# Optimization experiments

Measured on AMD Instinct MI355X. Metric: run time of the kernel, lower is better.

Reference implementation:

```python
import jax, jax.numpy as jnp
import numpy as np
import math

L, H, E, D = 4, 8, 256, 32  # layers, heads, embed, head_dim
SCALE = 1.0 / math.sqrt(D)

def _ln(x, w, b, eps=1e-5):
    mu = jnp.mean(x, -1, keepdims=True)
    var = jnp.mean((x - mu) ** 2, -1, keepdims=True)
    return (x - mu) * jax.lax.rsqrt(var + eps) * w + b

def setup_inputs() -> dict:
    key = jax.random.key(0)
    ks = jax.random.split(key, 16)
    B, S, C = 32, 512, 512
    w = lambda k, sh: jax.random.normal(k, sh, jnp.float32) * 0.05
    return {
        'cnn_features': jax.random.normal(ks[0], (B, S, C), jnp.float32),
        'cnn_w': w(ks[1], (E, C)), 'cnn_b': jnp.zeros((E,), jnp.float32),
        'tok_emb': w(ks[2], (2, E)),
        'Wq': w(ks[3], (L, E, E)), 'bq': jnp.zeros((L, E), jnp.float32),
        'Wk': w(ks[4], (L, E, E)), 'bk': jnp.zeros((L, E), jnp.float32),
        'Wv': w(ks[5], (L, E, E)), 'bv': jnp.zeros((L, E), jnp.float32),
        'Wo': w(ks[6], (L, E, E)), 'bo': jnp.zeros((L, E), jnp.float32),
        'ln1_w': jnp.ones((L, E), jnp.float32), 'ln1_b': jnp.zeros((L, E), jnp.float32),
        'ln2_w': jnp.ones((L, E), jnp.float32), 'ln2_b': jnp.zeros((L, E), jnp.float32),
        'mlp_w1': w(ks[7], (L, 3 * E, E)), 'mlp_b1': jnp.zeros((L, 3 * E), jnp.float32),
        'mlp_w2': w(ks[8], (L, E, 3 * E)), 'mlp_b2': jnp.zeros((L, E), jnp.float32),
        'lnf_w': jnp.ones((E,), jnp.float32), 'lnf_b': jnp.zeros((E,), jnp.float32),
        'out_w1': w(ks[9], (2 * E, E)), 'out_b1': jnp.zeros((2 * E,), jnp.float32),
        'out_w2': w(ks[10], (C, 2 * E)), 'out_b2': jnp.zeros((C,), jnp.float32),
    }

def _forward(cnn_features, cnn_w, cnn_b, tok_emb, Wq, bq, Wk, bk, Wv, bv, Wo, bo,
             ln1_w, ln1_b, ln2_w, ln2_b, mlp_w1, mlp_b1, mlp_w2, mlp_b2,
             lnf_w, lnf_b, out_w1, out_b1, out_w2, out_b2):
    B, S, _ = cnn_features.shape
    # CNN feature projection + token-type embedding (all tokens type 0)
    x = cnn_features @ cnn_w.T + cnn_b + tok_emb[0]  # [B,S,E]
    for i in range(L):
        q = (x @ Wq[i].T + bq[i]).reshape(B, S, H, D).transpose(0, 2, 1, 3)
        k = (x @ Wk[i].T + bk[i]).reshape(B, S, H, D).transpose(0, 2, 1, 3)
        v = (x @ Wv[i].T + bv[i]).reshape(B, S, H, D).transpose(0, 2, 1, 3)
        scores = jnp.einsum('bhqd,bhkd->bhqk', q, k) * SCALE
        attn = jax.nn.softmax(scores, axis=-1)  # dropout = identity (eval)
        attended = jnp.einsum('bhqk,bhkd->bhqd', attn, v)
        attended = attended.transpose(0, 2, 1, 3).reshape(B, S, E)
        attn_out = attended @ Wo[i].T + bo[i]
        x = _ln(x + attn_out, ln1_w[i], ln1_b[i])
        h = jax.nn.gelu(x @ mlp_w1[i].T + mlp_b1[i], approximate=False)
        mlp_out = h @ mlp_w2[i].T + mlp_b2[i]
        x = _ln(x + mlp_out, ln2_w[i], ln2_b[i])
    x = _ln(x, lnf_w, lnf_b)
    h = jax.nn.gelu(x @ out_w1.T + out_b1, approximate=False)
    out = jax.nn.relu(h @ out_w2.T + out_b2)  # [B,S,cnn_feature_dim]
    return out

def reference(cnn_features, cnn_w, cnn_b, tok_emb, Wq, bq, Wk, bk, Wv, bv, Wo, bo,
              ln1_w, ln1_b, ln2_w, ln2_b, mlp_w1, mlp_b1, mlp_w2, mlp_b2,
              lnf_w, lnf_b, out_w1, out_b1, out_w2, out_b2):
    return _forward(cnn_features, cnn_w, cnn_b, tok_emb, Wq, bq, Wk, bk, Wv, bv, Wo, bo,
                    ln1_w, ln1_b, ln2_w, ln2_b, mlp_w1, mlp_b1, mlp_w2, mlp_b2,
                    lnf_w, lnf_b, out_w1, out_b1, out_w2, out_b2)
```

## Files before the change

kernel.cpp:

```cpp
#include <hip/hip_runtime.h>
#include <hip/hip_bf16.h>
#include <math.h>

#define B_SZ 32
#define S_SZ 512
#define C_SZ 512
#define E_SZ 256
#define H_SZ 8
#define D_SZ 32
#define L_SZ 4
#define N_TOK (B_SZ * S_SZ)
#define HID 768
#define MB (1048576)

typedef __attribute__((ext_vector_type(8))) short bf16x8;
typedef __attribute__((ext_vector_type(4))) float f32x4_t;

__device__ __forceinline__ float gelu_f(float x) {
    return 0.5f * x * (1.0f + erff(x * 0.70710678118654752f));
}

__device__ __forceinline__ ushort f2bf(float f) {
    uint u = __float_as_uint(f);
    return (ushort)((u + 0x7FFFu + ((u >> 16) & 1u)) >> 16);
}
__device__ __forceinline__ uint pack2(float a, float b) {
    __hip_bfloat162 h = __float22bfloat162_rn(make_float2(a, b));
    union { __hip_bfloat162 h; uint u; } c; c.h = h;
    return c.u;
}
__device__ __forceinline__ void unpack8(uint4 u, float* f) {
    f[0] = __uint_as_float((u.x & 0xFFFFu) << 16); f[1] = __uint_as_float(u.x & 0xFFFF0000u);
    f[2] = __uint_as_float((u.y & 0xFFFFu) << 16); f[3] = __uint_as_float(u.y & 0xFFFF0000u);
    f[4] = __uint_as_float((u.z & 0xFFFFu) << 16); f[5] = __uint_as_float(u.z & 0xFFFF0000u);
    f[6] = __uint_as_float((u.w & 0xFFFFu) << 16); f[7] = __uint_as_float(u.w & 0xFFFF0000u);
}

__device__ __forceinline__ void gload16(const ushort* g, ushort* l) {
    __builtin_amdgcn_global_load_lds(
        (const __attribute__((address_space(1))) void*)g,
        (__attribute__((address_space(3))) void*)l, 16, 0, 0);
}

__global__ __launch_bounds__(256)
void cvt_kernel(const float* __restrict__ src, ushort* __restrict__ dst)
{
    const int i = (blockIdx.x * 256 + threadIdx.x) * 8;
    const float4 a = *(const float4*)(src + i);
    const float4 b = *(const float4*)(src + i + 4);
    uint4 o;
    o.x = pack2(a.x, a.y); o.y = pack2(a.z, a.w);
    o.z = pack2(b.x, b.y); o.w = pack2(b.z, b.w);
    *(uint4*)(dst + i) = o;
}

__global__ __launch_bounds__(256)
void wcvt_kernel(const float* __restrict__ cnn_w, const float* __restrict__ Wo,
                 const float* __restrict__ Wq, const float* __restrict__ Wk,
                 const float* __restrict__ Wv, const float* __restrict__ mw1,
                 const float* __restrict__ mw2, const float* __restrict__ ow1,
                 const float* __restrict__ ow2, ushort* __restrict__ wb)
{
    const int i = (blockIdx.x * 256 + threadIdx.x) * 8;
    const float* src;
    if (i < 131072)       src = cnn_w + i;
    else if (i < 393216)  src = Wo + (i - 131072);
    else if (i < 1179648) {
        const int r = i - 393216;
        const int layer = r / 196608, rem = r % 196608;
        const int sub = rem >> 16, off = rem & 65535;
        src = (sub == 0 ? Wq : sub == 1 ? Wk : Wv) + layer * 65536 + off;
    }
    else if (i < 1966080) src = mw1 + (i - 1179648);
    else if (i < 2752512) src = mw2 + (i - 1966080);
    else if (i < 2883584) src = ow1 + (i - 2752512);
    else                  src = ow2 + (i - 2883584);
    const float4 a = *(const float4*)src;
    const float4 b = *(const float4*)(src + 4);
    uint4 o;
    o.x = pack2(a.x, a.y); o.y = pack2(a.z, a.w);
    o.z = pack2(b.x, b.y); o.w = pack2(b.z, b.w);
    *(uint4*)(wb + i) = o;
}

__global__ __launch_bounds__(256)
void bqkv_kernel(const float* __restrict__ bq, const float* __restrict__ bk,
                 const float* __restrict__ bv, float* __restrict__ dst)
{
    const int idx = blockIdx.x * 256 + threadIdx.x;
    const int layer = idx / 768, j = idx % 768;
    float v = (j < 256) ? bq[layer * 256 + j]
            : (j < 512) ? bk[layer * 256 + j - 256]
                        : bv[layer * 256 + j - 512];
    dst[layer * 768 + j] = v;
}

template<int ACT, int EPI, bool OF, bool OB>
__global__ __launch_bounds__(256)
void gemm_bf16_kernel(const ushort* __restrict__ A, const ushort* __restrict__ W,
                      const float* __restrict__ bias, const float* __restrict__ bias2,
                      float* __restrict__ Cf, ushort* __restrict__ Cb,
                      ushort* __restrict__ Cb2, int M, int K, int F)
{
    __shared__ __align__(16) ushort As[2][128 * 64];
    __shared__ __align__(16) ushort Bs[2][64 * 64];
    const int tid = threadIdx.x;
    const int bm = blockIdx.x * 128, bn = blockIdx.y * 64;
    const int lane = tid & 63, w = tid >> 6;
    const int lr8 = lane >> 3, lseg = lane & 7;
    const int lsx = lseg ^ lr8;
    const int wm = w >> 1, wn = w & 1;
    const int fr = lane & 15, fk = lane >> 4;
    const int fx = fr & 7;
    f32x4_t acc[4][2] = {};

    const ushort* Ag = A + (size_t)(bm + w * 32 + lr8) * K + lsx * 8;
    const ushort* Wg = W + (size_t)(bn + w * 16 + lr8) * K + lsx * 8;

    #pragma unroll
    for (int q = 0; q < 4; ++q) gload16(Ag + (size_t)q * 8 * K, &As[0][(w * 32 + q * 8) * 64]);
    #pragma unroll
    for (int q = 0; q < 2; ++q) gload16(Wg + (size_t)q * 8 * K, &Bs[0][(w * 16 + q * 8) * 64]);
    __syncthreads();

    const int NT = K >> 6;
    int cur = 0;
    for (int t = 0; t < NT; ++t) {
        if (t + 1 < NT) {
            const size_t k0 = (size_t)(t + 1) << 6;
            #pragma unroll
            for (int q = 0; q < 4; ++q)
                gload16(Ag + (size_t)q * 8 * K + k0, &As[cur ^ 1][(w * 32 + q * 8) * 64]);
            #pragma unroll
            for (int q = 0; q < 2; ++q)
                gload16(Wg + (size_t)q * 8 * K + k0, &Bs[cur ^ 1][(w * 16 + q * 8) * 64]);
        }
        bf16x8 af[2][4], bw[2][2];
        #pragma unroll
        for (int kk = 0; kk < 2; ++kk) {
            const int rs = ((kk * 4 + fk) ^ fx) * 8;
            #pragma unroll
            for (int i = 0; i < 4; ++i)
                af[kk][i] = *(const bf16x8*)&As[cur][(wm * 64 + i * 16 + fr) * 64 + rs];
            #pragma unroll
            for (int j = 0; j < 2; ++j)
                bw[kk][j] = *(const bf16x8*)&Bs[cur][(wn * 32 + j * 16 + fr) * 64 + rs];
        }
        #pragma unroll
        for (int kk = 0; kk < 2; ++kk)
            #pragma unroll
            for (int i = 0; i < 4; ++i)
                #pragma unroll
                for (int j = 0; j < 2; ++j)
                    acc[i][j] = __builtin_amdgcn_mfma_f32_16x16x32_bf16(af[kk][i], bw[kk][j], acc[i][j], 0, 0, 0);
        __syncthreads();
        cur ^= 1;
    }

    #pragma unroll
    for (int j = 0; j < 2; ++j) {
        const int col = bn + wn * 32 + j * 16 + fr;
        float bb = bias[col];
        if (bias2) bb += bias2[col];
        #pragma unroll
        for (int i = 0; i < 4; ++i) {
            #pragma unroll
            for (int r = 0; r < 4; ++r) {
                const int row = bm + wm * 64 + i * 16 + fk * 4 + r;
                float t = acc[i][j][r] + bb;
                if (ACT == 1) t = gelu_f(t);
                if (ACT == 2) t = fmaxf(t, 0.0f);
                if (EPI == 1) {
                    const int b2 = row >> 9, s2 = row & 511;
                    if (col < 512) {
                        Cb[(size_t)row * 512 + col] = f2bf(t);
                    } else {
                        const int cc = col - 512;
                        Cb2[(size_t)(((b2 << 3) + (cc >> 5)) << 14) + ((cc & 31) << 9) + s2] = f2bf(t);
                    }
                } else {
                    if (OF) Cf[(size_t)row * F + col] = t;
                    if (OB) Cb[(size_t)row * F + col] = f2bf(t);
                }
            }
        }
    }
}

__global__ __launch_bounds__(512)
void gemm_ln_kernel(const ushort* __restrict__ A, const ushort* __restrict__ W,
                    const float* __restrict__ bias, float* __restrict__ x,
                    ushort* __restrict__ xb, const float* __restrict__ lnw,
                    const float* __restrict__ lnb, int K)
{
    __shared__ __align__(16) ushort As[2][64 * 64];
    __shared__ __align__(16) ushort Bs[2][256 * 64];
    __shared__ float psum[64][8], psq[64][8], murs[64][2];
    const int tid = threadIdx.x;
    const int bm = blockIdx.x * 64;
    const int lane = tid & 63, w = tid >> 6;
    const int lr8 = lane >> 3, lseg = lane & 7;
    const int lsx = lseg ^ lr8;
    const int fr = lane & 15, fk = lane >> 4;
    const int fx = fr & 7;
    f32x4_t acc[4][2] = {};

    const ushort* Ag = A + (size_t)(bm + w * 8 + lr8) * K + lsx * 8;
    const ushort* Wg = W + (size_t)(w * 32 + lr8) * K + lsx * 8;

    gload16(Ag, &As[0][(w * 8) * 64]);
    #pragma unroll
    for (int q = 0; q < 4; ++q) gload16(Wg + (size_t)q * 8 * K, &Bs[0][(w * 32 + q * 8) * 64]);
    __syncthreads();

    const int NT = K >> 6;
    int cur = 0;
    for (int t = 0; t < NT; ++t) {
        if (t + 1 < NT) {
            const size_t k0 = (size_t)(t + 1) << 6;
            gload16(Ag + k0, &As[cur ^ 1][(w * 8) * 64]);
            #pragma unroll
            for (int q = 0; q < 4; ++q)
                gload16(Wg + (size_t)q * 8 * K + k0, &Bs[cur ^ 1][(w * 32 + q * 8) * 64]);
        }
        bf16x8 af[2][4], bw[2][2];
        #pragma unroll
        for (int kk = 0; kk < 2; ++kk) {
            const int rs = ((kk * 4 + fk) ^ fx) * 8;
            #pragma unroll
            for (int i = 0; i < 4; ++i)
                af[kk][i] = *(const bf16x8*)&As[cur][(i * 16 + fr) * 64 + rs];
            #pragma unroll
            for (int j = 0; j < 2; ++j)
                bw[kk][j] = *(const bf16x8*)&Bs[cur][(w * 32 + j * 16 + fr) * 64 + rs];
        }
        #pragma unroll
        for (int kk = 0; kk < 2; ++kk)
            #pragma unroll
            for (int i = 0; i < 4; ++i)
                #pragma unroll
                for (int j = 0; j < 2; ++j)
                    acc[i][j] = __builtin_amdgcn_mfma_f32_16x16x32_bf16(af[kk][i], bw[kk][j], acc[i][j], 0, 0, 0);
        __syncthreads();
        cur ^= 1;
    }

    float y[4][2][4];
    #pragma unroll
    for (int j = 0; j < 2; ++j) {
        const int col = w * 32 + j * 16 + fr;
        const float bb = bias[col];
        #pragma unroll
        for (int i = 0; i < 4; ++i)
            #pragma unroll
            for (int r = 0; r < 4; ++r) {
                const int row = i * 16 + fk * 4 + r;
                y[i][j][r] = acc[i][j][r] + bb + x[(size_t)(bm + row) * 256 + col];
            }
    }
    #pragma unroll
    for (int i = 0; i < 4; ++i)
        #pragma unroll
        for (int r = 0; r < 4; ++r) {
            float s = y[i][0][r] + y[i][1][r];
            float q = y[i][0][r] * y[i][0][r] + y[i][1][r] * y[i][1][r];
            #pragma unroll
            for (int off = 1; off < 16; off <<= 1) {
                s += __shfl_xor(s, off);
                q += __shfl_xor(q, off);
            }
            if (fr == 0) {
                psum[i * 16 + fk * 4 + r][w] = s;
                psq [i * 16 + fk * 4 + r][w] = q;
            }
        }
    __syncthreads();
    if (tid < 64) {
        float ms = 0.f, mq = 0.f;
        #pragma unroll
        for (int ww = 0; ww < 8; ++ww) { ms += psum[tid][ww]; mq += psq[tid][ww]; }
        const float mu = ms * (1.0f / 256.0f);
        const float var = mq * (1.0f / 256.0f) - mu * mu;
        murs[tid][0] = mu;
        murs[tid][1] = rsqrtf(var + 1e-5f);
    }
    __syncthreads();
    #pragma unroll
    for (int i = 0; i < 4; ++i)
        #pragma unroll
        for (int r = 0; r < 4; ++r) {
            const int row = i * 16 + fk * 4 + r;
            const float mu = murs[row][0], rs = murs[row][1];
            #pragma unroll
            for (int j = 0; j < 2; ++j) {
                const int col = w * 32 + j * 16 + fr;
                const float xn = (y[i][j][r] - mu) * rs * lnw[col] + lnb[col];
                x [(size_t)(bm + row) * 256 + col] = xn;
                xb[(size_t)(bm + row) * 256 + col] = f2bf(xn);
            }
        }
}

__global__ __launch_bounds__(512)
void attn_v4(const ushort* __restrict__ qk, const ushort* __restrict__ vt,
             ushort* __restrict__ out)
{
    __shared__ __align__(16) ushort Ks[512 * 40];
    __shared__ __align__(16) ushort Vs[32 * 520];
    const int bh = blockIdx.x;
    const int b = bh >> 3, h = bh & 7;
    const int tid = threadIdx.x;
    const int w = tid >> 6, lane = tid & 63;
    const int g = lane >> 4, c = lane & 15;

    #pragma unroll
    for (int i = 0; i < 4; ++i) {
        const int idx = tid + i * 512;
        const int kr = idx >> 2, seg = idx & 3;
        const uint4 kv = *(const uint4*)(qk + ((size_t)b * 512 + kr) * 512
                                         + 256 + h * 32 + seg * 8);
        const int p = (((kr >> 2) & 1) << 4) | (((kr >> 3) & 3) << 2) | (kr & 3);
        const int pos = (kr & ~31) | p;
        *(uint4*)&Ks[pos * 40 + seg * 8] = kv;
        const int dr = idx >> 6, vseg = idx & 63;
        const uint4 vv = *(const uint4*)(vt + (size_t)bh * 16384 + dr * 512 + vseg * 8);
        *(uint4*)&Vs[dr * 520 + vseg * 8] = vv;
    }

    bf16x8 qf[4];
    #pragma unroll
    for (int j = 0; j < 4; ++j) {
        const size_t qrow = (size_t)b * 512 + (j * 8 + w) * 16 + c;
        const uint4 qv = *(const uint4*)(qk + qrow * 512 + h * 32 + g * 8);
        float f[8]; unpack8(qv, f);
        const float scale = 0.17677669529663689f;
        union { uint u[4]; bf16x8 v; } qq;
        #pragma unroll
        for (int t = 0; t < 4; ++t) qq.u[t] = pack2(f[2*t] * scale, f[2*t+1] * scale);
        qf[j] = qq.v;
    }
    __syncthreads();

    const f32x4_t zz = {0.f, 0.f, 0.f, 0.f};
    #pragma unroll
    for (int j = 0; j < 4; ++j) {
        float m = -INFINITY, l = 0.f;
        f32x4_t o0 = zz, o1 = zz;
        for (int kt = 0; kt < 4; ++kt) {
            const int kbase = kt * 128;
            f32x4_t s[8];
            __builtin_amdgcn_s_setprio(1);
            #pragma unroll
            for (int kf = 0; kf < 8; ++kf) {
                const bf16x8 kfrag = *(const bf16x8*)&Ks[(kbase + kf * 16 + c) * 40 + g * 8];
                s[kf] = __builtin_amdgcn_mfma_f32_16x16x32_bf16(kfrag, qf[j], zz, 0, 0, 0);
            }
            __builtin_amdgcn_s_setprio(0);

            float mt = s[0][0];
            #pragma unroll
            for (int kf = 0; kf < 8; ++kf)
                #pragma unroll
                for (int r = 0; r < 4; ++r) mt = fmaxf(mt, s[kf][r]);
            mt = fmaxf(mt, __shfl_xor(mt, 16));
            mt = fmaxf(mt, __shfl_xor(mt, 32));
            const float mn = fmaxf(m, mt);
            const float corr = __expf(m - mn);
            m = mn;
            float lt = 0.f;
            #pragma unroll
            for (int kf = 0; kf < 8; ++kf)
                #pragma unroll
                for (int r = 0; r < 4; ++r) {
                    const float p = __expf(s[kf][r] - mn);
                    s[kf][r] = p; lt += p;
                }
            lt += __shfl_xor(lt, 16);
            lt += __shfl_xor(lt, 32);
            l = l * corr + lt;
            #pragma unroll
            for (int r = 0; r < 4; ++r) { o0[r] *= corr; o1[r] *= corr; }

            #pragma unroll
            for (int t = 0; t < 4; ++t) {
                union { uint u[4]; bf16x8 v; } pf;
                pf.u[0] = pack2(s[2*t][0],   s[2*t][1]);
                pf.u[1] = pack2(s[2*t][2],   s[2*t][3]);
                pf.u[2] = pack2(s[2*t+1][0], s[2*t+1][1]);
                pf.u[3] = pack2(s[2*t+1][2], s[2*t+1][3]);
                const bf16x8 va0 = *(const bf16x8*)&Vs[c * 520 + kbase + t * 32 + g * 8];
                const bf16x8 va1 = *(const bf16x8*)&Vs[(16 + c) * 520 + kbase + t * 32 + g * 8];
                __builtin_amdgcn_s_setprio(1);
                o0 = __builtin_amdgcn_mfma_f32_16x16x32_bf16(va0, pf.v, o0, 0, 0, 0);
                o1 = __builtin_amdgcn_mfma_f32_16x16x32_bf16(va1, pf.v, o1, 0, 0, 0);
                __builtin_amdgcn_s_setprio(0);
            }
        }

        const float inv = 1.0f / l;
        const size_t obase = ((size_t)b * 512 + (j * 8 + w) * 16 + c) * 256 + h * 32;
        ushort4 w0, w1;
        w0.x = f2bf(o0[0] * inv); w0.y = f2bf(o0[1] * inv);
        w0.z = f2bf(o0[2] * inv); w0.w = f2bf(o0[3] * inv);
        w1.x = f2bf(o1[0] * inv); w1.y = f2bf(o1[1] * inv);
        w1.z = f2bf(o1[2] * inv); w1.w = f2bf(o1[3] * inv);
        *(ushort4*)(out + obase + g * 4)      = w0;
        *(ushort4*)(out + obase + 16 + g * 4) = w1;
    }
}

__global__ __launch_bounds__(256)
void lnf_kernel(const float* __restrict__ x, const float* __restrict__ w,
                const float* __restrict__ b, ushort* __restrict__ xb)
{
    const int lane = threadIdx.x & 63;
    const int wv = threadIdx.x >> 6;
    const size_t row = (size_t)blockIdx.x * 4 + wv;
    const float4 val = *(const float4*)(x + row * E_SZ + lane * 4);
    float s  = val.x + val.y + val.z + val.w;
    float ss = val.x * val.x + val.y * val.y + val.z * val.z + val.w * val.w;
    #pragma unroll
    for (int off = 1; off < 64; off <<= 1) {
        s  += __shfl_xor(s, off, 64);
        ss += __shfl_xor(ss, off, 64);
    }
    const float mu  = s * (1.0f / 256.0f);
    const float var = ss * (1.0f / 256.0f) - mu * mu;
    const float rs  = rsqrtf(var + 1e-5f);
    const float4 wv4 = *(const float4*)(w + lane * 4);
    const float4 bv4 = *(const float4*)(b + lane * 4);
    ushort4 ob;
    ob.x = f2bf((val.x - mu) * rs * wv4.x + bv4.x);
    ob.y = f2bf((val.y - mu) * rs * wv4.y + bv4.y);
    ob.z = f2bf((val.z - mu) * rs * wv4.z + bv4.z);
    ob.w = f2bf((val.w - mu) * rs * wv4.w + bv4.w);
    *(ushort4*)(xb + row * E_SZ + lane * 4) = ob;
}

extern "C" void kernel_launch(void* const* d_in, const int* in_sizes, int n_in,
                              void* d_out, int out_size, void* d_ws, size_t ws_size,
                              hipStream_t stream)
{
    const float* cnn   = (const float*)d_in[0];
    const float* cnn_w = (const float*)d_in[1];
    const float* cnn_b = (const float*)d_in[2];
    const float* tok   = (const float*)d_in[3];
    const float* Wq    = (const float*)d_in[4];
    const float* bq    = (const float*)d_in[5];
    const float* Wk    = (const float*)d_in[6];
    const float* bk    = (const float*)d_in[7];
    const float* Wv    = (const float*)d_in[8];
    const float* bv    = (const float*)d_in[9];
    const float* Wo    = (const float*)d_in[10];
    const float* bo    = (const float*)d_in[11];
    const float* ln1w  = (const float*)d_in[12];
    const float* ln1b  = (const float*)d_in[13];
    const float* ln2w  = (const float*)d_in[14];
    const float* ln2b  = (const float*)d_in[15];
    const float* mw1   = (const float*)d_in[16];
    const float* mb1   = (const float*)d_in[17];
    const float* mw2   = (const float*)d_in[18];
    const float* mb2   = (const float*)d_in[19];
    const float* lnfw  = (const float*)d_in[20];
    const float* lnfb  = (const float*)d_in[21];
    const float* ow1   = (const float*)d_in[22];
    const float* ob1   = (const float*)d_in[23];
    const float* ow2   = (const float*)d_in[24];
    const float* ob2   = (const float*)d_in[25];

    const int M = N_TOK;
    char* ws = (char*)d_ws;

    float*  x     = (float*)(ws + 0);
    ushort* xb    = (ushort*)(ws + 16 * MB);
    ushort* qkb   = (ushort*)(ws + 24 * MB);
    ushort* cnnb  = (ushort*)(ws + 24 * MB);
    ushort* vt    = (ushort*)(ws + 40 * MB);
    ushort* ab_   = (ushort*)(ws + 48 * MB);
    ushort* hb_   = (ushort*)(ws + 40 * MB);
    ushort* wb    = (ushort*)(ws + 64 * MB);

    ushort* cnn_wb = wb;
    ushort* Wob    = wb + 131072;
    ushort* wqkv   = wb + 393216;
    ushort* mw1b   = wb + 1179648;
    ushort* mw2b   = wb + 1966080;
    ushort* ow1b   = wb + 2752512;
    ushort* ow2b   = wb + 2883584;
    float*  bqkv   = (float*)(ws + 64 * MB + 6291456);

    cvt_kernel<<<dim3(4096), dim3(256), 0, stream>>>(cnn, cnnb);
    wcvt_kernel<<<dim3(1536), dim3(256), 0, stream>>>(
        cnn_w, Wo, Wq, Wk, Wv, mw1, mw2, ow1, ow2, wb);
    bqkv_kernel<<<dim3(12), dim3(256), 0, stream>>>(bq, bk, bv, bqkv);

    gemm_bf16_kernel<0, 0, true, true><<<dim3(M / 128, E_SZ / 64), dim3(256), 0, stream>>>(
        cnnb, cnn_wb, cnn_b, tok, x, xb, nullptr, M, C_SZ, E_SZ);

    for (int i = 0; i < L_SZ; ++i) {
        gemm_bf16_kernel<0, 1, false, false><<<dim3(M / 128, HID / 64), dim3(256), 0, stream>>>(
            xb, wqkv + (size_t)i * 196608, bqkv + (size_t)i * 768, nullptr,
            nullptr, qkb, vt, M, E_SZ, HID);

        attn_v4<<<dim3(B_SZ * H_SZ), dim3(512), 0, stream>>>(qkb, vt, ab_);

        gemm_ln_kernel<<<dim3(M / 64), dim3(512), 0, stream>>>(
            ab_, Wob + (size_t)i * 65536, bo + (size_t)i * E_SZ,
            x, xb, ln1w + (size_t)i * E_SZ, ln1b + (size_t)i * E_SZ, E_SZ);

        gemm_bf16_kernel<1, 0, false, true><<<dim3(M / 128, HID / 64), dim3(256), 0, stream>>>(
            xb, mw1b + (size_t)i * HID * E_SZ, mb1 + (size_t)i * HID, nullptr,
            nullptr, hb_, nullptr, M, E_SZ, HID);

        gemm_ln_kernel<<<dim3(M / 64), dim3(512), 0, stream>>>(
            hb_, mw2b + (size_t)i * E_SZ * HID, mb2 + (size_t)i * E_SZ,
            x, xb, ln2w + (size_t)i * E_SZ, ln2b + (size_t)i * E_SZ, HID);
    }

    lnf_kernel<<<dim3(M / 4), dim3(256), 0, stream>>>(x, lnfw, lnfb, xb);

    gemm_bf16_kernel<1, 0, false, true><<<dim3(M / 128, (2 * E_SZ) / 64), dim3(256), 0, stream>>>(
        xb, ow1b, ob1, nullptr, nullptr, hb_, nullptr, M, E_SZ, 2 * E_SZ);
    gemm_bf16_kernel<2, 0, true, false><<<dim3(M / 128, C_SZ / 64), dim3(256), 0, stream>>>(
        hb_, ow2b, ob2, nullptr, (float*)d_out, nullptr, nullptr, M, 2 * E_SZ, C_SZ);
}
```

Measured before the change: 522.7 us.

## Enlarge GEMM tiles, fuse final LayerNorm, split attention queries, merge setup kernels

Combines the three setup conversion kernels into one launch and widens the generic GEMM tile from 128x64 to 128x128 for more operand reuse per block. The final LayerNorm is fused into the last MLP gemm_ln kernel, removing a separate pass over x. Attention now splits queries into two chunks per (batch, head) to double the block count, and uses exp2 with a log2e-folded scale. Risks include higher register and LDS use from the larger tile, and duplicated K/V staging across the query chunks.

```diff
diff --git a/kernel.cpp b/kernel.cpp
--- a/kernel.cpp
+++ b/kernel.cpp
@@ -43,84 +43,82 @@
 }
 
 __global__ __launch_bounds__(256)
-void cvt_kernel(const float* __restrict__ src, ushort* __restrict__ dst)
+void setup_kernel(const float* __restrict__ cnn, const float* __restrict__ cnn_w,
+                  const float* __restrict__ Wo, const float* __restrict__ Wq,
+                  const float* __restrict__ Wk, const float* __restrict__ Wv,
+                  const float* __restrict__ mw1, const float* __restrict__ mw2,
+                  const float* __restrict__ ow1, const float* __restrict__ ow2,
+                  const float* __restrict__ bq, const float* __restrict__ bk,
+                  const float* __restrict__ bv, ushort* __restrict__ cnnb,
+                  ushort* __restrict__ wb, float* __restrict__ bqkv)
 {
-    const int i = (blockIdx.x * 256 + threadIdx.x) * 8;
-    const float4 a = *(const float4*)(src + i);
-    const float4 b = *(const float4*)(src + i + 4);
-    uint4 o;
-    o.x = pack2(a.x, a.y); o.y = pack2(a.z, a.w);
-    o.z = pack2(b.x, b.y); o.w = pack2(b.z, b.w);
-    *(uint4*)(dst + i) = o;
-}
-
-__global__ __launch_bounds__(256)
-void wcvt_kernel(const float* __restrict__ cnn_w, const float* __restrict__ Wo,
-                 const float* __restrict__ Wq, const float* __restrict__ Wk,
-                 const float* __restrict__ Wv, const float* __restrict__ mw1,
-                 const float* __restrict__ mw2, const float* __restrict__ ow1,
-                 const float* __restrict__ ow2, ushort* __restrict__ wb)
-{
-    const int i = (blockIdx.x * 256 + threadIdx.x) * 8;
-    const float* src;
-    if (i < 131072)       src = cnn_w + i;
-    else if (i < 393216)  src = Wo + (i - 131072);
-    else if (i < 1179648) {
-        const int r = i - 393216;
-        const int layer = r / 196608, rem = r % 196608;
-        const int sub = rem >> 16, off = rem & 65535;
-        src = (sub == 0 ? Wq : sub == 1 ? Wk : Wv) + layer * 65536 + off;
-    }
-    else if (i < 1966080) src = mw1 + (i - 1179648);
-    else if (i < 2752512) src = mw2 + (i - 1966080);
-    else if (i < 2883584) src = ow1 + (i - 2752512);
-    else                  src = ow2 + (i - 2883584);
-    const float4 a = *(const float4*)src;
-    const float4 b = *(const float4*)(src + 4);
-    uint4 o;
-    o.x = pack2(a.x, a.y); o.y = pack2(a.z, a.w);
-    o.z = pack2(b.x, b.y); o.w = pack2(b.z, b.w);
-    *(uint4*)(wb + i) = o;
-}
-
-__global__ __launch_bounds__(256)
-void bqkv_kernel(const float* __restrict__ bq, const float* __restrict__ bk,
-                 const float* __restrict__ bv, float* __restrict__ dst)
-{
-    const int idx = blockIdx.x * 256 + threadIdx.x;
-    const int layer = idx / 768, j = idx % 768;
-    float v = (j < 256) ? bq[layer * 256 + j]
-            : (j < 512) ? bk[layer * 256 + j - 256]
-                        : bv[layer * 256 + j - 512];
-    dst[layer * 768 + j] = v;
+    const int bid = blockIdx.x, tid = threadIdx.x;
+    if (bid < 4096) {
+        const int i = (bid * 256 + tid) * 8;
+        const float4 a = *(const float4*)(cnn + i);
+        const float4 b = *(const float4*)(cnn + i + 4);
+        uint4 o;
+        o.x = pack2(a.x, a.y); o.y = pack2(a.z, a.w);
+        o.z = pack2(b.x, b.y); o.w = pack2(b.z, b.w);
+        *(uint4*)(cnnb + i) = o;
+    } else if (bid < 5632) {
+        const int i = ((bid - 4096) * 256 + tid) * 8;
+        const float* src;
+        if (i < 131072)       src = cnn_w + i;
+        else if (i < 393216)  src = Wo + (i - 131072);
+        else if (i < 1179648) {
+            const int r = i - 393216;
+            const int layer = r / 196608, rem = r % 196608;
+            const int sub = rem >> 16, off = rem & 65535;
+            src = (sub == 0 ? Wq : sub == 1 ? Wk : Wv) + layer * 65536 + off;
+        }
+        else if (i < 1966080) src = mw1 + (i - 1179648);
+        else if (i < 2752512) src = mw2 + (i - 1966080);
+        else if (i < 2883584) src = ow1 + (i - 2752512);
+        else                  src = ow2 + (i - 2883584);
+        const float4 a = *(const float4*)src;
+        const float4 b = *(const float4*)(src + 4);
+        uint4 o;
+        o.x = pack2(a.x, a.y); o.y = pack2(a.z, a.w);
+        o.z = pack2(b.x, b.y); o.w = pack2(b.z, b.w);
+        *(uint4*)(wb + i) = o;
+    } else {
+        const int idx = (bid - 5632) * 256 + tid;
+        const int layer = idx / 768, j = idx % 768;
+        float v = (j < 256) ? bq[layer * 256 + j]
+                : (j < 512) ? bk[layer * 256 + j - 256]
+                            : bv[layer * 256 + j - 512];
+        bqkv[layer * 768 + j] = v;
+    }
 }
 
 template<int ACT, int EPI, bool OF, bool OB>
 __global__ __launch_bounds__(256)
-void gemm_bf16_kernel(const ushort* __restrict__ A, const ushort* __restrict__ W,
-                      const float* __restrict__ bias, const float* __restrict__ bias2,
-                      float* __restrict__ Cf, ushort* __restrict__ Cb,
-                      ushort* __restrict__ Cb2, int M, int K, int F)
+void gemm128_kernel(const ushort* __restrict__ A, const ushort* __restrict__ W,
+                    const float* __restrict__ bias, const float* __restrict__ bias2,
+                    float* __restrict__ Cf, ushort* __restrict__ Cb,
+                    ushort* __restrict__ Cb2, int M, int K, int F)
 {
     __shared__ __align__(16) ushort As[2][128 * 64];
-    __shared__ __align__(16) ushort Bs[2][64 * 64];
+    __shared__ __align__(16) ushort Bs[2][128 * 64];
     const int tid = threadIdx.x;
-    const int bm = blockIdx.x * 128, bn = blockIdx.y * 64;
+    const int bm = blockIdx.x * 128, bn = blockIdx.y * 128;
     const int lane = tid & 63, w = tid >> 6;
     const int lr8 = lane >> 3, lseg = lane & 7;
     const int lsx = lseg ^ lr8;
     const int wm = w >> 1, wn = w & 1;
     const int fr = lane & 15, fk = lane >> 4;
     const int fx = fr & 7;
-    f32x4_t acc[4][2] = {};
+    f32x4_t acc[4][4] = {};
 
     const ushort* Ag = A + (size_t)(bm + w * 32 + lr8) * K + lsx * 8;
-    const ushort* Wg = W + (size_t)(bn + w * 16 + lr8) * K + lsx * 8;
-
-    #pragma unroll
-    for (int q = 0; q < 4; ++q) gload16(Ag + (size_t)q * 8 * K, &As[0][(w * 32 + q * 8) * 64]);
-    #pragma unroll
-    for (int q = 0; q < 2; ++q) gload16(Wg + (size_t)q * 8 * K, &Bs[0][(w * 16 + q * 8) * 64]);
+    const ushort* Wg = W + (size_t)(bn + w * 32 + lr8) * K + lsx * 8;
+
+    #pragma unroll
+    for (int q = 0; q < 4; ++q) {
+        gload16(Ag + (size_t)q * 8 * K, &As[0][(w * 32 + q * 8) * 64]);
+        gload16(Wg + (size_t)q * 8 * K, &Bs[0][(w * 32 + q * 8) * 64]);
+    }
     __syncthreads();
 
     const int NT = K >> 6;
@@ -129,37 +127,34 @@
         if (t + 1 < NT) {
             const size_t k0 = (size_t)(t + 1) << 6;
             #pragma unroll
-            for (int q = 0; q < 4; ++q)
+            for (int q = 0; q < 4; ++q) {
                 gload16(Ag + (size_t)q * 8 * K + k0, &As[cur ^ 1][(w * 32 + q * 8) * 64]);
-            #pragma unroll
-            for (int q = 0; q < 2; ++q)
-                gload16(Wg + (size_t)q * 8 * K + k0, &Bs[cur ^ 1][(w * 16 + q * 8) * 64]);
-        }
-        bf16x8 af[2][4], bw[2][2];
+                gload16(Wg + (size_t)q * 8 * K + k0, &Bs[cur ^ 1][(w * 32 + q * 8) * 64]);
+            }
+        }
         #pragma unroll
         for (int kk = 0; kk < 2; ++kk) {
             const int rs = ((kk * 4 + fk) ^ fx) * 8;
+            bf16x8 af[4], bw[4];
             #pragma unroll
             for (int i = 0; i < 4; ++i)
-                af[kk][i] = *(const bf16x8*)&As[cur][(wm * 64 + i * 16 + fr) * 64 + rs];
-            #pragma unroll
-            for (int j = 0; j < 2; ++j)
-                bw[kk][j] = *(const bf16x8*)&Bs[cur][(wn * 32 + j * 16 + fr) * 64 + rs];
-        }
-        #pragma unroll
-        for (int kk = 0; kk < 2; ++kk)
+                af[i] = *(const bf16x8*)&As[cur][(wm * 64 + i * 16 + fr) * 64 + rs];
+            #pragma unroll
+            for (int j = 0; j < 4; ++j)
+                bw[j] = *(const bf16x8*)&Bs[cur][(wn * 64 + j * 16 + fr) * 64 + rs];
             #pragma unroll
             for (int i = 0; i < 4; ++i)
                 #pragma unroll
-                for (int j = 0; j < 2; ++j)
-                    acc[i][j] = __builtin_amdgcn_mfma_f32_16x16x32_bf16(af[kk][i], bw[kk][j], acc[i][j], 0, 0, 0);
+                for (int j = 0; j < 4; ++j)
+                    acc[i][j] = __builtin_amdgcn_mfma_f32_16x16x32_bf16(af[i], bw[j], acc[i][j], 0, 0, 0);
+        }
         __syncthreads();
         cur ^= 1;
     }
 
     #pragma unroll
-    for (int j = 0; j < 2; ++j) {
-        const int col = bn + wn * 32 + j * 16 + fr;
+    for (int j = 0; j < 4; ++j) {
+        const int col = bn + wn * 64 + j * 16 + fr;
         float bb = bias[col];
         if (bias2) bb += bias2[col];
         #pragma unroll
@@ -187,11 +182,13 @@
     }
 }
 
+template<bool FINAL>
 __global__ __launch_bounds__(512)
 void gemm_ln_kernel(const ushort* __restrict__ A, const ushort* __restrict__ W,
                     const float* __restrict__ bias, float* __restrict__ x,
                     ushort* __restrict__ xb, const float* __restrict__ lnw,
-                    const float* __restrict__ lnb, int K)
+                    const float* __restrict__ lnb, const float* __restrict__ lnfw,
+                    const float* __restrict__ lnfb, int K)
 {
     __shared__ __align__(16) ushort As[2][64 * 64];
     __shared__ __align__(16) ushort Bs[2][256 * 64];
@@ -295,19 +292,64 @@
             for (int j = 0; j < 2; ++j) {
                 const int col = w * 32 + j * 16 + fr;
                 const float xn = (y[i][j][r] - mu) * rs * lnw[col] + lnb[col];
-                x [(size_t)(bm + row) * 256 + col] = xn;
-                xb[(size_t)(bm + row) * 256 + col] = f2bf(xn);
-            }
-        }
+                y[i][j][r] = xn;
+                if (!FINAL) {
+                    x [(size_t)(bm + row) * 256 + col] = xn;
+                    xb[(size_t)(bm + row) * 256 + col] = f2bf(xn);
+                }
+            }
+        }
+    if (FINAL) {
+        #pragma unroll
+        for (int i = 0; i < 4; ++i)
+            #pragma unroll
+            for (int r = 0; r < 4; ++r) {
+                float s = y[i][0][r] + y[i][1][r];
+                float q = y[i][0][r] * y[i][0][r] + y[i][1][r] * y[i][1][r];
+                #pragma unroll
+                for (int off = 1; off < 16; off <<= 1) {
+                    s += __shfl_xor(s, off);
+                    q += __shfl_xor(q, off);
+                }
+                if (fr == 0) {
+                    psum[i * 16 + fk * 4 + r][w] = s;
+                    psq [i * 16 + fk * 4 + r][w] = q;
+                }
+            }
+        __syncthreads();
+        if (tid < 64) {
+            float ms = 0.f, mq = 0.f;
+            #pragma unroll
+            for (int ww = 0; ww < 8; ++ww) { ms += psum[tid][ww]; mq += psq[tid][ww]; }
+            const float mu = ms * (1.0f / 256.0f);
+            const float var = mq * (1.0f / 256.0f) - mu * mu;
+            murs[tid][0] = mu;
+            murs[tid][1] = rsqrtf(var + 1e-5f);
+        }
+        __syncthreads();
+        #pragma unroll
+        for (int i = 0; i < 4; ++i)
+            #pragma unroll
+            for (int r = 0; r < 4; ++r) {
+                const int row = i * 16 + fk * 4 + r;
+                const float mu = murs[row][0], rs = murs[row][1];
+                #pragma unroll
+                for (int j = 0; j < 2; ++j) {
+                    const int col = w * 32 + j * 16 + fr;
+                    const float xn = (y[i][j][r] - mu) * rs * lnfw[col] + lnfb[col];
+                    xb[(size_t)(bm + row) * 256 + col] = f2bf(xn);
+                }
+            }
+    }
 }
 
 __global__ __launch_bounds__(512)
-void attn_v4(const ushort* __restrict__ qk, const ushort* __restrict__ vt,
+void attn_v5(const ushort* __restrict__ qk, const ushort* __restrict__ vt,
              ushort* __restrict__ out)
 {
     __shared__ __align__(16) ushort Ks[512 * 40];
     __shared__ __align__(16) ushort Vs[32 * 520];
-    const int bh = blockIdx.x;
+    const int bh = blockIdx.x, qc = blockIdx.y;
     const int b = bh >> 3, h = bh & 7;
     const int tid = threadIdx.x;
     const int w = tid >> 6, lane = tid & 63;
@@ -327,13 +369,13 @@
         *(uint4*)&Vs[dr * 520 + vseg * 8] = vv;
     }
 
-    bf16x8 qf[4];
-    #pragma unroll
-    for (int j = 0; j < 4; ++j) {
-        const size_t qrow = (size_t)b * 512 + (j * 8 + w) * 16 + c;
+    bf16x8 qf[2];
+    #pragma unroll
+    for (int j = 0; j < 2; ++j) {
+        const size_t qrow = (size_t)b * 512 + qc * 256 + (j * 8 + w) * 16 + c;
         const uint4 qv = *(const uint4*)(qk + qrow * 512 + h * 32 + g * 8);
         float f[8]; unpack8(qv, f);
-        const float scale = 0.17677669529663689f;
+        const float scale = 0.25506806865756986f;
         union { uint u[4]; bf16x8 v; } qq;
         #pragma unroll
         for (int t = 0; t < 4; ++t) qq.u[t] = pack2(f[2*t] * scale, f[2*t+1] * scale);
@@ -343,7 +385,7 @@
 
     const f32x4_t zz = {0.f, 0.f, 0.f, 0.f};
     #pragma unroll
-    for (int j = 0; j < 4; ++j) {
+    for (int j = 0; j < 2; ++j) {
         float m = -INFINITY, l = 0.f;
         f32x4_t o0 = zz, o1 = zz;
         for (int kt = 0; kt < 4; ++kt) {
@@ -365,14 +407,14 @@
             mt = fmaxf(mt, __shfl_xor(mt, 16));
             mt = fmaxf(mt, __shfl_xor(mt, 32));
             const float mn = fmaxf(m, mt);
-            const float corr = __expf(m - mn);
+            const float corr = exp2f(m - mn);
             m = mn;
             float lt = 0.f;
             #pragma unroll
             for (int kf = 0; kf < 8; ++kf)
                 #pragma unroll
                 for (int r = 0; r < 4; ++r) {
-                    const float p = __expf(s[kf][r] - mn);
+                    const float p = exp2f(s[kf][r] - mn);
                     s[kf][r] = p; lt += p;
                 }
             lt += __shfl_xor(lt, 16);
@@ -398,7 +440,7 @@
         }
 
         const float inv = 1.0f / l;
-        const size_t obase = ((size_t)b * 512 + (j * 8 + w) * 16 + c) * 256 + h * 32;
+        const size_t obase = ((size_t)b * 512 + qc * 256 + (j * 8 + w) * 16 + c) * 256 + h * 32;
         ushort4 w0, w1;
         w0.x = f2bf(o0[0] * inv); w0.y = f2bf(o0[1] * inv);
         w0.z = f2bf(o0[2] * inv); w0.w = f2bf(o0[3] * inv);
@@ -407,34 +449,6 @@
         *(ushort4*)(out + obase + g * 4)      = w0;
         *(ushort4*)(out + obase + 16 + g * 4) = w1;
     }
-}
-
-__global__ __launch_bounds__(256)
-void lnf_kernel(const float* __restrict__ x, const float* __restrict__ w,
-                const float* __restrict__ b, ushort* __restrict__ xb)
-{
-    const int lane = threadIdx.x & 63;
-    const int wv = threadIdx.x >> 6;
-    const size_t row = (size_t)blockIdx.x * 4 + wv;
-    const float4 val = *(const float4*)(x + row * E_SZ + lane * 4);
-    float s  = val.x + val.y + val.z + val.w;
-    float ss = val.x * val.x + val.y * val.y + val.z * val.z + val.w * val.w;
-    #pragma unroll
-    for (int off = 1; off < 64; off <<= 1) {
-        s  += __shfl_xor(s, off, 64);
-        ss += __shfl_xor(ss, off, 64);
-    }
-    const float mu  = s * (1.0f / 256.0f);
-    const float var = ss * (1.0f / 256.0f) - mu * mu;
-    const float rs  = rsqrtf(var + 1e-5f);
-    const float4 wv4 = *(const float4*)(w + lane * 4);
-    const float4 bv4 = *(const float4*)(b + lane * 4);
-    ushort4 ob;
-    ob.x = f2bf((val.x - mu) * rs * wv4.x + bv4.x);
-    ob.y = f2bf((val.y - mu) * rs * wv4.y + bv4.y);
-    ob.z = f2bf((val.z - mu) * rs * wv4.z + bv4.z);
-    ob.w = f2bf((val.w - mu) * rs * wv4.w + bv4.w);
-    *(ushort4*)(xb + row * E_SZ + lane * 4) = ob;
 }
 
 extern "C" void kernel_launch(void* const* d_in, const int* in_sizes, int n_in,
@@ -489,38 +503,44 @@
     ushort* ow2b   = wb + 2883584;
     float*  bqkv   = (float*)(ws + 64 * MB + 6291456);
 
-    cvt_kernel<<<dim3(4096), dim3(256), 0, stream>>>(cnn, cnnb);
-    wcvt_kernel<<<dim3(1536), dim3(256), 0, stream>>>(
-        cnn_w, Wo, Wq, Wk, Wv, mw1, mw2, ow1, ow2, wb);
-    bqkv_kernel<<<dim3(12), dim3(256), 0, stream>>>(bq, bk, bv, bqkv);
-
-    gemm_bf16_kernel<0, 0, true, true><<<dim3(M / 128, E_SZ / 64), dim3(256), 0, stream>>>(
+    setup_kernel<<<dim3(5644), dim3(256), 0, stream>>>(
+        cnn, cnn_w, Wo, Wq, Wk, Wv, mw1, mw2, ow1, ow2, bq, bk, bv,
+        cnnb, wb, bqkv);
+
+    gemm128_kernel<0, 0, true, true><<<dim3(M / 128, E_SZ / 128), dim3(256), 0, stream>>>(
         cnnb, cnn_wb, cnn_b, tok, x, xb, nullptr, M, C_SZ, E_SZ);
 
     for (int i = 0; i < L_SZ; ++i) {
-        gemm_bf16_kernel<0, 1, false, false><<<dim3(M / 128, HID / 64), dim3(256), 0, stream>>>(
+        gemm128_kernel<0, 1, false, false><<<dim3(M / 128, HID / 128), dim3(256), 0, stream>>>(
             xb, wqkv + (size_t)i * 196608, bqkv + (size_t)i * 768, nullptr,
             nullptr, qkb, vt, M, E_SZ, HID);
 
-        attn_v4<<<dim3(B_SZ * H_SZ), dim3(512), 0, stream>>>(qkb, vt, ab_);
-
-        gemm_ln_kernel<<<dim3(M / 64), dim3(512), 0, stream>>>(
+        attn_v5<<<dim3(B_SZ * H_SZ, 2), dim3(512), 0, stream>>>(qkb, vt, ab_);
+
+        gemm_ln_kernel<false><<<dim3(M / 64), dim3(512), 0, stream>>>(
             ab_, Wob + (size_t)i * 65536, bo + (size_t)i * E_SZ,
-            x, xb, ln1w + (size_t)i * E_SZ, ln1b + (size_t)i * E_SZ, E_SZ);
-
-        gemm_bf16_kernel<1, 0, false, true><<<dim3(M / 128, HID / 64), dim3(256), 0, stream>>>(
+            x, xb, ln1w + (size_t)i * E_SZ, ln1b + (size_t)i * E_SZ,
+            nullptr, nullptr, E_SZ);
+
+        gemm128_kernel<1, 0, false, true><<<dim3(M / 128, HID / 128), dim3(256), 0, stream>>>(
             xb, mw1b + (size_t)i * HID * E_SZ, mb1 + (size_t)i * HID, nullptr,
             nullptr, hb_, nullptr, M, E_SZ, HID);
 
-        gemm_ln_kernel<<<dim3(M / 64), dim3(512), 0, stream>>>(
-            hb_, mw2b + (size_t)i * E_SZ * HID, mb2 + (size_t)i * E_SZ,
-            x, xb, ln2w + (size_t)i * E_SZ, ln2b + (size_t)i * E_SZ, HID);
-    }
-
-    lnf_kernel<<<dim3(M / 4), dim3(256), 0, stream>>>(x, lnfw, lnfb, xb);
-
-    gemm_bf16_kernel<1, 0, false, true><<<dim3(M / 128, (2 * E_SZ) / 64), dim3(256), 0, stream>>>(
+        if (i < L_SZ - 1) {
+            gemm_ln_kernel<false><<<dim3(M / 64), dim3(512), 0, stream>>>(
+                hb_, mw2b + (size_t)i * E_SZ * HID, mb2 + (size_t)i * E_SZ,
+                x, xb, ln2w + (size_t)i * E_SZ, ln2b + (size_t)i * E_SZ,
+                nullptr, nullptr, HID);
+        } else {
+            gemm_ln_kernel<true><<<dim3(M / 64), dim3(512), 0, stream>>>(
+                hb_, mw2b + (size_t)i * E_SZ * HID, mb2 + (size_t)i * E_SZ,
+                x, xb, ln2w + (size_t)i * E_SZ, ln2b + (size_t)i * E_SZ,
+                lnfw, lnfb, HID);
+        }
+    }
+
+    gemm128_kernel<1, 0, false, true><<<dim3(M / 128, (2 * E_SZ) / 128), dim3(256), 0, stream>>>(
         xb, ow1b, ob1, nullptr, nullptr, hb_, nullptr, M, E_SZ, 2 * E_SZ);
-    gemm_bf16_kernel<2, 0, true, false><<<dim3(M / 128, C_SZ / 64), dim3(256), 0, stream>>>(
+    gemm128_kernel<2, 0, true, false><<<dim3(M / 128, C_SZ / 128), dim3(256), 0, stream>>>(
         hb_, ow2b, ob2, nullptr, (float*)d_out, nullptr, nullptr, M, 2 * E_SZ, C_SZ);
 }
```

New measurement: 591.5 us. +13.2%, slower.
